# Optimization experiments

Measured on AMD Instinct MI355X. Metric: run time of the kernel, lower is better.

The kernel has to match this reference:

```python
import jax, jax.numpy as jnp
import numpy as np

B, N, P, K, E = 4, 20000, 128, 128, 160000


def setup_inputs() -> dict:
    key = jax.random.key(0)
    ks = jax.random.split(key, 16)
    inv_p = 1.0 / np.sqrt(P)
    inv_3p = 1.0 / np.sqrt(3 * P)
    return {
        "x_in": jax.random.normal(ks[0], (B, N, P), jnp.float32),
        "vertex_areas": jax.random.uniform(ks[1], (B, N), jnp.float32, 1e-3, 1.0),
        "evals": jax.random.uniform(ks[2], (B, K), jnp.float32, 0.0, 10.0),
        "evecs": jax.random.normal(ks[3], (B, N, K), jnp.float32),
        "gradX_vals": jax.random.normal(ks[4], (B, E), jnp.float32),
        "gradY_vals": jax.random.normal(ks[5], (B, E), jnp.float32),
        "grad_rows": jax.random.randint(ks[6], (B, E), 0, N, jnp.int32),
        "grad_cols": jax.random.randint(ks[7], (B, E), 0, N, jnp.int32),
        # learned params
        "diffusion_times": jax.random.uniform(ks[8], (P,), jnp.float32, 1e-3, 0.1),
        "B_re": jax.random.normal(ks[9], (P, P), jnp.float32) * inv_p,
        "B_im": jax.random.normal(ks[10], (P, P), jnp.float32) * inv_p,
        "W1": jax.random.normal(ks[11], (P, 3 * P), jnp.float32) * inv_3p,
        "b1": jnp.zeros((P,), jnp.float32),
        "W2": jax.random.normal(ks[12], (P, P), jnp.float32) * inv_p,
        "b2": jnp.zeros((P,), jnp.float32),
        "W3": jax.random.normal(ks[13], (P, P), jnp.float32) * inv_p,
        "b3": jnp.zeros((P,), jnp.float32),
    }


def _spmm(rows, cols, vals, x):
    # sparse (n,n) @ dense (n,p) via COO gather/scatter
    return jax.ops.segment_sum(vals[:, None] * x[cols], rows, num_segments=x.shape[0])


def reference(x_in, vertex_areas, evals, evecs, gradX_vals, gradY_vals,
              grad_rows, grad_cols, diffusion_times, B_re, B_im,
              W1, b1, W2, b2, W3, b3):
    # SpectralDiffusion: project -> spectral heat scaling -> unproject
    times = jnp.clip(diffusion_times, 1e-8)                       # (P,)
    x_spec = jnp.einsum('bnk,bnp->bkp', evecs, x_in * vertex_areas[..., None])
    scale = jnp.exp(-evals[..., None] * times[None, None, :])     # (B,K,P)
    x_diffuse = jnp.einsum('bnk,bkp->bnp', evecs, scale * x_spec)  # (B,N,P)

    # sparse gradient halves
    gx = jax.vmap(_spmm)(grad_rows, grad_cols, gradX_vals, x_diffuse)  # (B,N,P)
    gy = jax.vmap(_spmm)(grad_rows, grad_cols, gradY_vals, x_diffuse)

    # SpatialGradient: tanh(re*B_re(re) + im*B_im(im))
    x_grad_features = jnp.tanh(gx * (gx @ B_re.T) + gy * (gy @ B_im.T))

    # MiniMLP on concatenated features (dropout inactive in eval)
    h = jnp.concatenate([x_in, x_diffuse, x_grad_features], axis=-1)  # (B,N,3P)
    h = jax.nn.relu(h @ W1.T + b1)
    h = jax.nn.relu(h @ W2.T + b2)
    h = h @ W3.T + b3
    return h + x_in
```

## Files before the change

kernel.cpp:

```cpp
#include <hip/hip_runtime.h>
#include <hip/hip_bf16.h>
#include <cstddef>

#define B_ 4
#define N_ 20000
#define P_ 128
#define K_ 128
#define E_ 160000

constexpr int NCH_S = 79;
constexpr int NSCB  = 79;

typedef __attribute__((ext_vector_type(8))) short short8;
typedef __attribute__((ext_vector_type(4))) float f32x4;

__device__ __forceinline__ unsigned pk2(float x, float y) {
  __hip_bfloat162 h = __float22bfloat162_rn(make_float2(x, y));
  union { __hip_bfloat162 h; unsigned u; } c; c.h = h; return c.u;
}
__device__ __forceinline__ float bf2f(short s) {
  union { unsigned u; float f; } c; c.u = ((unsigned)(unsigned short)s) << 16; return c.f;
}

__global__ __launch_bounds__(256)
void k_prep(const float* __restrict__ ev, const float* __restrict__ xin,
            const float* __restrict__ areas,
            __hip_bfloat16* __restrict__ evT, __hip_bfloat16* __restrict__ xT)
{
  const int tn = blockIdx.x, half = blockIdx.y & 1, mat = blockIdx.y >> 1;
  const int b = blockIdx.z, t = threadIdx.x;
  const int n0 = tn * 64, c0 = half * 64;
  __shared__ float ld[64][65];
  const float* src = (mat ? xin : ev) + (size_t)b * N_ * 128;
  const float* ab  = areas + (size_t)b * N_;
#pragma unroll
  for (int i = 0; i < 4; ++i) {
    int gid = t + i * 256;
    int r = gid >> 4, c4 = (gid & 15) << 2;
    int n = n0 + r;
    float4 v = make_float4(0.f, 0.f, 0.f, 0.f);
    if (n < N_) {
      v = *(const float4*)(src + (size_t)n * 128 + c0 + c4);
      if (mat == 0) { float ar = ab[n]; v.x *= ar; v.y *= ar; v.z *= ar; v.w *= ar; }
    }
    ld[r][c4] = v.x; ld[r][c4+1] = v.y; ld[r][c4+2] = v.z; ld[r][c4+3] = v.w;
  }
  __syncthreads();
  __hip_bfloat16* dst = (mat ? xT : evT) + (size_t)b * 128 * N_;
#pragma unroll
  for (int i = 0; i < 4; ++i) {
    int gid = t + i * 256;
    int cr = gid >> 4, nq = (gid & 15) << 2;
    int n = n0 + nq;
    if (n + 4 <= N_) {
      uint2 u;
      u.x = pk2(ld[nq][cr],   ld[nq+1][cr]);
      u.y = pk2(ld[nq+2][cr], ld[nq+3][cr]);
      *(uint2*)(dst + (size_t)(c0 + cr) * N_ + n) = u;
    }
  }
}

__global__ __launch_bounds__(256)
void k_wprep(const float* __restrict__ Bre, const float* __restrict__ Bim,
             uint4* __restrict__ WfRe, uint4* __restrict__ WfIm)
{
  int fid = blockIdx.x * 256 + threadIdx.x;
  if (fid >= 2048) return;
  int gg = fid >> 7, rr = fid & 127;
  const float* s0 = Bre + rr * 128 + gg * 8;
  const float* s1 = Bim + rr * 128 + gg * 8;
  float4 a0 = *(const float4*)s0, a1 = *(const float4*)(s0 + 4);
  uint4 u; u.x = pk2(a0.x, a0.y); u.y = pk2(a0.z, a0.w);
  u.z = pk2(a1.x, a1.y); u.w = pk2(a1.z, a1.w);
  WfRe[fid] = u;
  float4 b0 = *(const float4*)s1, b1 = *(const float4*)(s1 + 4);
  uint4 v; v.x = pk2(b0.x, b0.y); v.y = pk2(b0.z, b0.w);
  v.z = pk2(b1.x, b1.y); v.w = pk2(b1.z, b1.w);
  WfIm[fid] = v;
}

__device__ __forceinline__ void stg64(uint4* __restrict__ Ls,
                                      const __hip_bfloat16* __restrict__ G,
                                      int n0, int t)
{
#pragma unroll
  for (int i = 0; i < 2; ++i) {
    int gid = t + i * 512;
    int r = gid >> 3, kg = gid & 7;
    int n = n0 + kg * 8;
    uint4 u = make_uint4(0u, 0u, 0u, 0u);
    if (n < N_) u = *(const uint4*)(G + (size_t)r * N_ + n);
    Ls[r * 8 + (kg ^ (r & 7))] = u;
  }
}

__global__ __launch_bounds__(512)
void k_spec_mm(const __hip_bfloat16* __restrict__ evT,
               const __hip_bfloat16* __restrict__ xT,
               float* __restrict__ part)
{
  const int c = blockIdx.x, b = blockIdx.y, t = threadIdx.x;
  const int l = t & 63, wid = t >> 6;
  const int wr = wid >> 2, wc = wid & 3;
  const int lr = l & 15, lg = l >> 4;
  __shared__ uint4 AsB[1024];
  __shared__ uint4 WsB[1024];
  f32x4 acc[4][2];
#pragma unroll
  for (int m = 0; m < 4; ++m)
#pragma unroll
    for (int n = 0; n < 2; ++n) acc[m][n] = (f32x4)0.f;

  const __hip_bfloat16* eb = evT + (size_t)b * 128 * N_;
  const __hip_bfloat16* xb = xT  + (size_t)b * 128 * N_;

  for (int s = 0; s < 4; ++s) {
    int n0 = c * 256 + s * 64;
    __syncthreads();
    stg64(AsB, eb, n0, t);
    stg64(WsB, xb, n0, t);
    __syncthreads();
    const short8* Ap = (const short8*)AsB;
    const short8* Wp = (const short8*)WsB;
#pragma unroll
    for (int kk = 0; kk < 2; ++kk) {
      int gg = kk * 4 + lg;
      short8 a[4], w[2];
#pragma unroll
      for (int m = 0; m < 4; ++m) { int rr = wr*64 + m*16 + lr; a[m] = Ap[rr*8 + (gg ^ (rr & 7))]; }
#pragma unroll
      for (int n = 0; n < 2; ++n) { int rr = wc*32 + n*16 + lr; w[n] = Wp[rr*8 + (gg ^ (rr & 7))]; }
#pragma unroll
      for (int m = 0; m < 4; ++m)
#pragma unroll
        for (int n = 0; n < 2; ++n)
          acc[m][n] = __builtin_amdgcn_mfma_f32_16x16x32_bf16(a[m], w[n], acc[m][n], 0, 0, 0);
    }
  }

  float* po = part + ((size_t)(b * NCH_S + c) << 14);
#pragma unroll
  for (int m = 0; m < 4; ++m)
#pragma unroll
    for (int r = 0; r < 4; ++r) {
      int row = wr*64 + m*16 + lg*4 + r;
#pragma unroll
      for (int n = 0; n < 2; ++n) {
        int col = wc*32 + n*16 + lr;
        po[row * 128 + col] = acc[m][n][r];
      }
    }
}

__global__ __launch_bounds__(256)
void k_spec_reduce(const float* __restrict__ partial, const float* __restrict__ evals,
                   const float* __restrict__ times, float* __restrict__ sspecT)
{
  int idx = blockIdx.x * 256 + threadIdx.x;
  int b = idx >> 14;
  int kp = idx & 16383;
  int k = kp >> 7, p = kp & 127;
  float s = 0.f;
  const float* pb = partial + (size_t)b * NCH_S * (K_*P_) + kp;
  for (int c = 0; c < NCH_S; ++c) s += pb[(size_t)c * (K_*P_)];
  float tt = times[p]; tt = tt < 1e-8f ? 1e-8f : tt;
  float sc = __expf(-evals[b*K_ + k] * tt);
  sspecT[((size_t)b*P_ + p) * K_ + k] = s * sc;
}

__device__ __forceinline__ void stg_f32(uint4* __restrict__ Ls, const float* __restrict__ G,
                                        int ld, int nrows, int t)
{
#pragma unroll
  for (int i = 0; i < 4; ++i) {
    int gid = t + i * 512;
    int r = gid >> 4, kg = gid & 15;
    float4 v0 = make_float4(0.f,0.f,0.f,0.f), v1 = v0;
    if (r < nrows) {
      const float* p = G + (size_t)r * ld + kg * 8;
      v0 = *(const float4*)p;
      v1 = *(const float4*)(p + 4);
    }
    uint4 u;
    u.x = pk2(v0.x, v0.y); u.y = pk2(v0.z, v0.w);
    u.z = pk2(v1.x, v1.y); u.w = pk2(v1.z, v1.w);
    Ls[r * 16 + (kg ^ (r & 7))] = u;
  }
}

__device__ __forceinline__ void stg_bf(uint4* __restrict__ Ls,
                                       const __hip_bfloat16* __restrict__ G,
                                       int ld, int nrows, int t)
{
#pragma unroll
  for (int i = 0; i < 4; ++i) {
    int gid = t + i * 512;
    int r = gid >> 4, kg = gid & 15;
    uint4 u = make_uint4(0u,0u,0u,0u);
    if (r < nrows) u = *(const uint4*)(G + (size_t)r * ld + kg * 8);
    Ls[r * 16 + (kg ^ (r & 7))] = u;
  }
}

__device__ __forceinline__ void mfma_chunk(const uint4* AsB, const uint4* WsB,
                                           int wr, int wc, int lr, int lg,
                                           f32x4 acc[4][2])
{
  const short8* Ap = (const short8*)AsB;
  const short8* Wp = (const short8*)WsB;
#pragma unroll
  for (int kk = 0; kk < 4; ++kk) {
    int gg = kk * 4 + lg;
    short8 a[4], w[2];
#pragma unroll
    for (int m = 0; m < 4; ++m) {
      int rr = wr*64 + m*16 + lr;
      a[m] = Ap[rr*16 + (gg ^ (rr & 7))];
    }
#pragma unroll
    for (int n = 0; n < 2; ++n) {
      int rr = wc*32 + n*16 + lr;
      w[n] = Wp[rr*16 + (gg ^ (rr & 7))];
    }
#pragma unroll
    for (int m = 0; m < 4; ++m)
#pragma unroll
      for (int n = 0; n < 2; ++n)
        acc[m][n] = __builtin_amdgcn_mfma_f32_16x16x32_bf16(a[m], w[n], acc[m][n], 0, 0, 0);
  }
}

template<int MODE>
__global__ __launch_bounds__(512)
void k_rowgemm(const void* __restrict__ A0, const void* __restrict__ A1,
               const void* __restrict__ A2, int abf,
               const float* __restrict__ W, int ldw, int wbs, int nchunk,
               const float* __restrict__ bias, const float* __restrict__ resid,
               void* __restrict__ C)
{
  const int b = blockIdx.y, r0 = blockIdx.x * 128, t = threadIdx.x;
  const int l = t & 63, wid = t >> 6;
  const int wr = wid >> 2, wc = wid & 3;
  const int lr = l & 15, lg = l >> 4;
  __shared__ uint4 AsB[2048];
  __shared__ uint4 WsB[2048];
  f32x4 acc[4][2];
#pragma unroll
  for (int m = 0; m < 4; ++m)
#pragma unroll
    for (int n = 0; n < 2; ++n) acc[m][n] = (f32x4)0.f;

  const float* Wb = W + (size_t)b * wbs;
  const int nrows = min(128, N_ - r0);
  const size_t aoff = (size_t)b * N_ * 128 + (size_t)r0 * 128;

  for (int kc = 0; kc < nchunk; ++kc) {
    const void* Av = (kc == 0 ? A0 : (kc == 1 ? A1 : A2));
    __syncthreads();
    if ((abf >> kc) & 1) stg_bf(AsB, (const __hip_bfloat16*)Av + aoff, 128, nrows, t);
    else                 stg_f32(AsB, (const float*)Av + aoff, 128, nrows, t);
    stg_f32(WsB, Wb + kc * 128, ldw, 128, t);
    __syncthreads();
    mfma_chunk(AsB, WsB, wr, wc, lr, lg, acc);
  }

  const size_t cb = (size_t)b * N_ * 128;
#pragma unroll
  for (int m = 0; m < 4; ++m) {
    int rowt = wr*64 + m*16 + lg*4;
#pragma unroll
    for (int r = 0; r < 4; ++r) {
      int row = r0 + rowt + r;
      if (row >= N_) continue;
#pragma unroll
      for (int n = 0; n < 2; ++n) {
        int col = wc*32 + n*16 + lr;
        float v = acc[m][n][r];
        if (MODE == 1 || MODE == 2) v = fmaxf(v + bias[col], 0.f);
        if (MODE == 3) {
          v += bias[col] + resid[cb + (size_t)row*128 + col];
          ((float*)C)[cb + (size_t)row*128 + col] = v;
        } else {
          ((__hip_bfloat16*)C)[cb + (size_t)row*128 + col] = __float2bfloat16(v);
        }
      }
    }
  }
}

__device__ __forceinline__ void stg64r(uint4* __restrict__ Ls,
                                       const __hip_bfloat16* __restrict__ G,
                                       int nrows, int t)
{
#pragma unroll
  for (int i = 0; i < 4; ++i) {
    int gid = t + i * 256;
    int r = gid >> 4, kg = gid & 15;
    uint4 u = make_uint4(0u,0u,0u,0u);
    if (r < nrows) u = *(const uint4*)(G + (size_t)r * 128 + kg * 8);
    Ls[r * 16 + (kg ^ (r & 7))] = u;
  }
}

__device__ __forceinline__ void mfma_pass64(const uint4* As, const uint4* __restrict__ Wf,
                                            int wc, int lr, int lg, f32x4 acc[4][2])
{
  const short8* Ap = (const short8*)As;
  const short8* Wp = (const short8*)Wf;
#pragma unroll
  for (int kk = 0; kk < 4; ++kk) {
    int gg = kk * 4 + lg;
    short8 a[4], w[2];
#pragma unroll
    for (int m = 0; m < 4; ++m) { int rr = m*16 + lr; a[m] = Ap[rr*16 + (gg ^ (rr & 7))]; }
#pragma unroll
    for (int n = 0; n < 2; ++n) { int rr = wc*32 + n*16 + lr; w[n] = Wp[(gg << 7) + rr]; }
#pragma unroll
    for (int m = 0; m < 4; ++m)
#pragma unroll
      for (int n = 0; n < 2; ++n)
        acc[m][n] = __builtin_amdgcn_mfma_f32_16x16x32_bf16(a[m], w[n], acc[m][n], 0, 0, 0);
  }
}

__global__ __launch_bounds__(256)
void k_grad(const uint4* __restrict__ WfRe, const uint4* __restrict__ WfIm,
            __hip_bfloat16* __restrict__ gx, const __hip_bfloat16* __restrict__ gy)
{
  const int b = blockIdx.y, r0 = blockIdx.x * 64, t = threadIdx.x;
  const int l = t & 63, wc = t >> 6;
  const int lr = l & 15, lg = l >> 4;
  __shared__ uint4 As[1024];
  f32x4 acc1[4][2], acc2[4][2];
#pragma unroll
  for (int m = 0; m < 4; ++m)
#pragma unroll
    for (int n = 0; n < 2; ++n) { acc1[m][n] = (f32x4)0.f; acc2[m][n] = (f32x4)0.f; }

  __hip_bfloat16*       gxb = gx + (size_t)b * N_ * P_;
  const __hip_bfloat16* gyb = gy + (size_t)b * N_ * P_;
  const int nrows = min(64, N_ - r0);

  stg64r(As, gxb + (size_t)r0 * 128, nrows, t);
  __syncthreads();
  mfma_pass64(As, WfRe, wc, lr, lg, acc1);
  __syncthreads();
  stg64r(As, gyb + (size_t)r0 * 128, nrows, t);
#pragma unroll
  for (int m = 0; m < 4; ++m)
#pragma unroll
    for (int r = 0; r < 4; ++r) {
      int row = r0 + m*16 + lg*4 + r;
      if (row >= N_) continue;
#pragma unroll
      for (int n = 0; n < 2; ++n) {
        int col = wc*32 + n*16 + lr;
        acc1[m][n][r] *= bf2f(*(const short*)(gxb + (size_t)row*128 + col));
      }
    }
  __syncthreads();
  mfma_pass64(As, WfIm, wc, lr, lg, acc2);

#pragma unroll
  for (int m = 0; m < 4; ++m)
#pragma unroll
    for (int r = 0; r < 4; ++r) {
      int row = r0 + m*16 + lg*4 + r;
      if (row >= N_) continue;
#pragma unroll
      for (int n = 0; n < 2; ++n) {
        int col = wc*32 + n*16 + lr;
        float g2 = bf2f(*(const short*)(gyb + (size_t)row*128 + col));
        float s = acc1[m][n][r] + g2 * acc2[m][n][r];
        s = fminf(fmaxf(s, -15.f), 15.f);
        float e = __expf(2.f * s);
        gxb[(size_t)row*128 + col] = __float2bfloat16((e - 1.f) / (e + 1.f));
      }
    }
}

__global__ void k_count(const int* __restrict__ rows, int* __restrict__ cnt)
{
  int b = blockIdx.y;
  int e = blockIdx.x * 256 + threadIdx.x;
  if (e < E_) atomicAdd(&cnt[b*N_ + rows[(size_t)b*E_ + e]], 1);
}

__global__ __launch_bounds__(256)
void k_scan_blk(const int* __restrict__ cnt, int* __restrict__ off,
                int* __restrict__ bsum)
{
  const int c = blockIdx.x, b = blockIdx.y, t = threadIdx.x;
  const int lane = t & 63, wid = t >> 6;
  __shared__ int wt[4];
  int i = c * 256 + t;
  int v = (i < N_) ? cnt[b*N_ + i] : 0;
  int x = v;
#pragma unroll
  for (int ofs = 1; ofs < 64; ofs <<= 1) {
    int y = __shfl_up(x, ofs, 64);
    if (lane >= ofs) x += y;
  }
  if (lane == 63) wt[wid] = x;
  __syncthreads();
  int wofs = 0;
  for (int wj = 0; wj < wid; ++wj) wofs += wt[wj];
  if (i < N_) off[b*(N_+1) + i] = wofs + x - v;
  if (t == 255) bsum[b*128 + c] = wofs + x;
}

__global__ __launch_bounds__(64)
void k_scan_top(int* __restrict__ bsum, int* __restrict__ off)
{
  const int b = blockIdx.x, t = threadIdx.x;
  int running = 0;
  for (int base = 0; base < 128; base += 64) {
    int i = base + t;
    int v = (i < NSCB) ? bsum[b*128 + i] : 0;
    int x = v;
#pragma unroll
    for (int ofs = 1; ofs < 64; ofs <<= 1) {
      int y = __shfl_up(x, ofs, 64);
      if (t >= ofs) x += y;
    }
    if (i < 128) bsum[b*128 + i] = running + x - v;
    running += __shfl(x, 63, 64);
  }
  if (t == 0) off[b*(N_+1) + N_] = running;
}

__global__ __launch_bounds__(256)
void k_scan_add(const int* __restrict__ bsum, int* __restrict__ off,
                int* __restrict__ pos)
{
  const int c = blockIdx.x, b = blockIdx.y;
  int i = c * 256 + (int)threadIdx.x;
  if (i < N_) {
    int o = off[b*(N_+1) + i] + bsum[b*128 + c];
    off[b*(N_+1) + i] = o;
    pos[b*N_ + i] = o;
  }
}

__global__ void k_fill(const int* __restrict__ rows, const int* __restrict__ cols,
                       const float* __restrict__ vx, const float* __restrict__ vy,
                       int* __restrict__ pos, uint4* __restrict__ prec)
{
  int b = blockIdx.y;
  int e = blockIdx.x * 256 + threadIdx.x;
  if (e < E_) {
    size_t be = (size_t)b*E_ + e;
    int r = rows[be];
    int p = atomicAdd(&pos[b*N_ + r], 1);
    if (p >= 0 && p < E_) {
      uint4 rec;
      rec.x = (unsigned)cols[be];
      rec.y = __float_as_uint(vx[be]);
      rec.z = __float_as_uint(vy[be]);
      rec.w = 0u;
      prec[(size_t)b*E_ + p] = rec;
    }
  }
}

__global__ __launch_bounds__(256)
void k_gather(const __hip_bfloat16* __restrict__ xd, const uint4* __restrict__ prec,
              const int* __restrict__ off,
              __hip_bfloat16* __restrict__ gx, __hip_bfloat16* __restrict__ gy)
{
  const int b = blockIdx.y;
  const int row = (blockIdx.x * 256 + threadIdx.x) >> 6;
  const int lane = threadIdx.x & 63;
  const int q = lane >> 4, ql = lane & 15;
  if (row >= N_) return;
  const int s = off[b*(N_+1) + row], e = off[b*(N_+1) + row + 1];
  float ax[8], ay[8];
#pragma unroll
  for (int k = 0; k < 8; ++k) { ax[k] = 0.f; ay[k] = 0.f; }
  const __hip_bfloat16* xdb = xd + (size_t)b * N_ * P_;
  const uint4* pb = prec + (size_t)b * E_;

  for (int i = s; i < e; i += 4) {
    int idx = i + q;
    bool valid = idx < e;
    uint4 rec = pb[valid ? idx : (e - 1)];
    float fx = valid ? __uint_as_float(rec.y) : 0.f;
    float fy = valid ? __uint_as_float(rec.z) : 0.f;
    uint4 v = *(const uint4*)(xdb + (size_t)rec.x * P_ + ql * 8);
    float x0 = __uint_as_float(v.x << 16), x1 = __uint_as_float(v.x & 0xffff0000u);
    float x2 = __uint_as_float(v.y << 16), x3 = __uint_as_float(v.y & 0xffff0000u);
    float x4 = __uint_as_float(v.z << 16), x5 = __uint_as_float(v.z & 0xffff0000u);
    float x6 = __uint_as_float(v.w << 16), x7 = __uint_as_float(v.w & 0xffff0000u);
    ax[0] = fmaf(fx, x0, ax[0]); ax[1] = fmaf(fx, x1, ax[1]);
    ax[2] = fmaf(fx, x2, ax[2]); ax[3] = fmaf(fx, x3, ax[3]);
    ax[4] = fmaf(fx, x4, ax[4]); ax[5] = fmaf(fx, x5, ax[5]);
    ax[6] = fmaf(fx, x6, ax[6]); ax[7] = fmaf(fx, x7, ax[7]);
    ay[0] = fmaf(fy, x0, ay[0]); ay[1] = fmaf(fy, x1, ay[1]);
    ay[2] = fmaf(fy, x2, ay[2]); ay[3] = fmaf(fy, x3, ay[3]);
    ay[4] = fmaf(fy, x4, ay[4]); ay[5] = fmaf(fy, x5, ay[5]);
    ay[6] = fmaf(fy, x6, ay[6]); ay[7] = fmaf(fy, x7, ay[7]);
  }
#pragma unroll
  for (int k = 0; k < 8; ++k) {
    ax[k] += __shfl_xor(ax[k], 16, 64); ax[k] += __shfl_xor(ax[k], 32, 64);
    ay[k] += __shfl_xor(ay[k], 16, 64); ay[k] += __shfl_xor(ay[k], 32, 64);
  }
  if (lane < 16) {
    size_t o = (size_t)b * N_ * P_ + (size_t)row * P_ + ql * 8;
    uint4 ux, uy;
    ux.x = pk2(ax[0], ax[1]); ux.y = pk2(ax[2], ax[3]);
    ux.z = pk2(ax[4], ax[5]); ux.w = pk2(ax[6], ax[7]);
    uy.x = pk2(ay[0], ay[1]); uy.y = pk2(ay[2], ay[3]);
    uy.z = pk2(ay[4], ay[5]); uy.w = pk2(ay[6], ay[7]);
    *(uint4*)(gx + o) = ux;
    *(uint4*)(gy + o) = uy;
  }
}

extern "C" void kernel_launch(void* const* d_in, const int* in_sizes, int n_in,
                              void* d_out, int out_size, void* d_ws, size_t ws_size,
                              hipStream_t stream)
{
  const float* x_in  = (const float*)d_in[0];
  const float* areas = (const float*)d_in[1];
  const float* evals = (const float*)d_in[2];
  const float* evecs = (const float*)d_in[3];
  const float* gXv   = (const float*)d_in[4];
  const float* gYv   = (const float*)d_in[5];
  const int*   grows = (const int*)d_in[6];
  const int*   gcols = (const int*)d_in[7];
  const float* times = (const float*)d_in[8];
  const float* Bre   = (const float*)d_in[9];
  const float* Bim   = (const float*)d_in[10];
  const float* W1    = (const float*)d_in[11];
  const float* b1    = (const float*)d_in[12];
  const float* W2    = (const float*)d_in[13];
  const float* b2    = (const float*)d_in[14];
  const float* W3    = (const float*)d_in[15];
  const float* b3    = (const float*)d_in[16];

  float* ws = (float*)d_ws;
  __hip_bfloat16* xd_bf = (__hip_bfloat16*)ws;
  float*          part  = ws + 6000000;
  __hip_bfloat16* gx_bf = (__hip_bfloat16*)(ws + 12000000);
  __hip_bfloat16* gy_bf = (__hip_bfloat16*)(ws + 18000000);
  __hip_bfloat16* evT   = gx_bf;
  __hip_bfloat16* xT    = gy_bf;

  uint4* prec   = (uint4*)(ws + 24000000);
  int*   ipos   = (int*)(ws + 26560000);
  int*   ioff   = ipos + B_*N_;
  float* sspecT = ws + 26750000;
  uint4* WfRe   = (uint4*)(ws + 26816000);
  uint4* WfIm   = WfRe + 2048;
  int*   bsum   = (int*)(WfIm + 2048);
  float* out    = (float*)d_out;

  const int GB = (N_ + 127) / 128;
  const int TN = (N_ + 63) / 64;

  k_prep<<<dim3(TN, 4, B_), 256, 0, stream>>>(evecs, x_in, areas, evT, xT);
  k_wprep<<<dim3(8), 256, 0, stream>>>(Bre, Bim, WfRe, WfIm);
  k_spec_mm<<<dim3(NCH_S, B_), 512, 0, stream>>>(evT, xT, part);
  k_spec_reduce<<<dim3(B_*K_*P_/256), 256, 0, stream>>>(part, evals, times, sspecT);
  k_rowgemm<0><<<dim3(GB, B_), 512, 0, stream>>>(evecs, nullptr, nullptr, 0, sspecT,
                                                 128, K_*P_, 1, nullptr, nullptr, xd_bf);
  hipMemsetAsync(ipos, 0, (size_t)B_*N_*sizeof(int), stream);
  k_count<<<dim3(E_/256, B_), 256, 0, stream>>>(grows, ipos);
  k_scan_blk<<<dim3(NSCB, B_), 256, 0, stream>>>(ipos, ioff, bsum);
  k_scan_top<<<dim3(B_), 64, 0, stream>>>(bsum, ioff);
  k_scan_add<<<dim3(NSCB, B_), 256, 0, stream>>>(bsum, ioff, ipos);
  k_fill<<<dim3(E_/256, B_), 256, 0, stream>>>(grows, gcols, gXv, gYv, ipos, prec);
  k_gather<<<dim3(N_/4, B_), 256, 0, stream>>>(xd_bf, prec, ioff, gx_bf, gy_bf);
  k_grad<<<dim3(TN, B_), 256, 0, stream>>>(WfRe, WfIm, gx_bf, gy_bf);
  k_rowgemm<1><<<dim3(GB, B_), 512, 0, stream>>>(x_in, xd_bf, gx_bf, 0b110, W1,
                                                 384, 0, 3, b1, nullptr, gy_bf);
  k_rowgemm<2><<<dim3(GB, B_), 512, 0, stream>>>(gy_bf, nullptr, nullptr, 1, W2,
                                                 128, 0, 1, b2, nullptr, gx_bf);
  k_rowgemm<3><<<dim3(GB, B_), 512, 0, stream>>>(gx_bf, nullptr, nullptr, 1, W3,
                                                 128, 0, 1, b3, x_in, out);
}
```

Measured before the change: 274.8 us.

## Fuse sparse gradient gather with spatial-gradient MFMA kernel via LDS staging

```diff
diff --git a/kernel.cpp b/kernel.cpp
--- a/kernel.cpp
+++ b/kernel.cpp
@@ -289,20 +289,6 @@
   }
 }
 
-__device__ __forceinline__ void stg64r(uint4* __restrict__ Ls,
-                                       const __hip_bfloat16* __restrict__ G,
-                                       int nrows, int t)
-{
-#pragma unroll
-  for (int i = 0; i < 4; ++i) {
-    int gid = t + i * 256;
-    int r = gid >> 4, kg = gid & 15;
-    uint4 u = make_uint4(0u,0u,0u,0u);
-    if (r < nrows) u = *(const uint4*)(G + (size_t)r * 128 + kg * 8);
-    Ls[r * 16 + (kg ^ (r & 7))] = u;
-  }
-}
-
 __device__ __forceinline__ void mfma_pass64(const uint4* As, const uint4* __restrict__ Wf,
                                             int wc, int lr, int lg, f32x4 acc[4][2])
 {
@@ -325,57 +311,95 @@
 }
 
 __global__ __launch_bounds__(256)
-void k_grad(const uint4* __restrict__ WfRe, const uint4* __restrict__ WfIm,
-            __hip_bfloat16* __restrict__ gx, const __hip_bfloat16* __restrict__ gy)
+void k_gather_grad(const __hip_bfloat16* __restrict__ xd, const uint4* __restrict__ prec,
+                   const int* __restrict__ off,
+                   const uint4* __restrict__ WfRe, const uint4* __restrict__ WfIm,
+                   __hip_bfloat16* __restrict__ xg)
 {
   const int b = blockIdx.y, r0 = blockIdx.x * 64, t = threadIdx.x;
-  const int l = t & 63, wc = t >> 6;
+  const int l = t & 63, w = t >> 6;
+  const int q = l >> 4, ql = l & 15;
+  __shared__ uint4 As[1024];
+  __shared__ uint4 As2[1024];
+  const __hip_bfloat16* xdb = xd + (size_t)b * N_ * P_;
+  const uint4* pb = prec + (size_t)b * E_;
+
+  for (int rr = 0; rr < 16; ++rr) {
+    const int lrow = w * 16 + rr;
+    const int row = r0 + lrow;
+    if (row < N_) {
+      const int s = off[b*(N_+1) + row], e = off[b*(N_+1) + row + 1];
+      float ax[8], ay[8];
+#pragma unroll
+      for (int k = 0; k < 8; ++k) { ax[k] = 0.f; ay[k] = 0.f; }
+      for (int i = s; i < e; i += 4) {
+        int idx = i + q;
+        bool valid = idx < e;
+        uint4 rec = pb[valid ? idx : (e - 1)];
+        float fx = valid ? __uint_as_float(rec.y) : 0.f;
+        float fy = valid ? __uint_as_float(rec.z) : 0.f;
+        uint4 v = *(const uint4*)(xdb + (size_t)rec.x * P_ + ql * 8);
+        float x0 = __uint_as_float(v.x << 16), x1 = __uint_as_float(v.x & 0xffff0000u);
+        float x2 = __uint_as_float(v.y << 16), x3 = __uint_as_float(v.y & 0xffff0000u);
+        float x4 = __uint_as_float(v.z << 16), x5 = __uint_as_float(v.z & 0xffff0000u);
+        float x6 = __uint_as_float(v.w << 16), x7 = __uint_as_float(v.w & 0xffff0000u);
+        ax[0] = fmaf(fx, x0, ax[0]); ax[1] = fmaf(fx, x1, ax[1]);
+        ax[2] = fmaf(fx, x2, ax[2]); ax[3] = fmaf(fx, x3, ax[3]);
+        ax[4] = fmaf(fx, x4, ax[4]); ax[5] = fmaf(fx, x5, ax[5]);
+        ax[6] = fmaf(fx, x6, ax[6]); ax[7] = fmaf(fx, x7, ax[7]);
+        ay[0] = fmaf(fy, x0, ay[0]); ay[1] = fmaf(fy, x1, ay[1]);
+        ay[2] = fmaf(fy, x2, ay[2]); ay[3] = fmaf(fy, x3, ay[3]);
+        ay[4] = fmaf(fy, x4, ay[4]); ay[5] = fmaf(fy, x5, ay[5]);
+        ay[6] = fmaf(fy, x6, ay[6]); ay[7] = fmaf(fy, x7, ay[7]);
+      }
+#pragma unroll
+      for (int k = 0; k < 8; ++k) {
+        ax[k] += __shfl_xor(ax[k], 16, 64); ax[k] += __shfl_xor(ax[k], 32, 64);
+        ay[k] += __shfl_xor(ay[k], 16, 64); ay[k] += __shfl_xor(ay[k], 32, 64);
+      }
+      if (l < 16) {
+        int sidx = lrow * 16 + (ql ^ (lrow & 7));
+        uint4 ux, uy;
+        ux.x = pk2(ax[0], ax[1]); ux.y = pk2(ax[2], ax[3]);
+        ux.z = pk2(ax[4], ax[5]); ux.w = pk2(ax[6], ax[7]);
+        uy.x = pk2(ay[0], ay[1]); uy.y = pk2(ay[2], ay[3]);
+        uy.z = pk2(ay[4], ay[5]); uy.w = pk2(ay[6], ay[7]);
+        As[sidx] = ux;
+        As2[sidx] = uy;
+      }
+    }
+  }
+  __syncthreads();
+
   const int lr = l & 15, lg = l >> 4;
-  __shared__ uint4 As[1024];
   f32x4 acc1[4][2], acc2[4][2];
 #pragma unroll
   for (int m = 0; m < 4; ++m)
 #pragma unroll
     for (int n = 0; n < 2; ++n) { acc1[m][n] = (f32x4)0.f; acc2[m][n] = (f32x4)0.f; }
-
-  __hip_bfloat16*       gxb = gx + (size_t)b * N_ * P_;
-  const __hip_bfloat16* gyb = gy + (size_t)b * N_ * P_;
-  const int nrows = min(64, N_ - r0);
-
-  stg64r(As, gxb + (size_t)r0 * 128, nrows, t);
-  __syncthreads();
-  mfma_pass64(As, WfRe, wc, lr, lg, acc1);
-  __syncthreads();
-  stg64r(As, gyb + (size_t)r0 * 128, nrows, t);
+  mfma_pass64(As,  WfRe, w, lr, lg, acc1);
+  mfma_pass64(As2, WfIm, w, lr, lg, acc2);
+
+  const short* S1 = (const short*)As;
+  const short* S2 = (const short*)As2;
+  __hip_bfloat16* xgb = xg + (size_t)b * N_ * P_;
 #pragma unroll
   for (int m = 0; m < 4; ++m)
 #pragma unroll
     for (int r = 0; r < 4; ++r) {
-      int row = r0 + m*16 + lg*4 + r;
+      int rowt = m*16 + lg*4 + r;
+      int row = r0 + rowt;
       if (row >= N_) continue;
 #pragma unroll
       for (int n = 0; n < 2; ++n) {
-        int col = wc*32 + n*16 + lr;
-        acc1[m][n][r] *= bf2f(*(const short*)(gxb + (size_t)row*128 + col));
-      }
-    }
-  __syncthreads();
-  mfma_pass64(As, WfIm, wc, lr, lg, acc2);
-
-#pragma unroll
-  for (int m = 0; m < 4; ++m)
-#pragma unroll
-    for (int r = 0; r < 4; ++r) {
-      int row = r0 + m*16 + lg*4 + r;
-      if (row >= N_) continue;
-#pragma unroll
-      for (int n = 0; n < 2; ++n) {
-        int col = wc*32 + n*16 + lr;
-        float g2 = bf2f(*(const short*)(gyb + (size_t)row*128 + col));
-        float s = acc1[m][n][r] + g2 * acc2[m][n][r];
+        int col = w*32 + n*16 + lr;
+        int gidx = (rowt*16 + ((col>>3) ^ (rowt & 7)))*8 + (col & 7);
+        float g1 = bf2f(S1[gidx]);
+        float g2 = bf2f(S2[gidx]);
+        float s = g1 * acc1[m][n][r] + g2 * acc2[m][n][r];
         s = fminf(fmaxf(s, -15.f), 15.f);
         float e = __expf(2.f * s);
-        gxb[(size_t)row*128 + col] = __float2bfloat16((e - 1.f) / (e + 1.f));
+        xgb[(size_t)row*128 + col] = __float2bfloat16((e - 1.f) / (e + 1.f));
       }
     }
 }
@@ -461,60 +485,6 @@
       rec.w = 0u;
       prec[(size_t)b*E_ + p] = rec;
     }
-  }
-}
-
-__global__ __launch_bounds__(256)
-void k_gather(const __hip_bfloat16* __restrict__ xd, const uint4* __restrict__ prec,
-              const int* __restrict__ off,
-              __hip_bfloat16* __restrict__ gx, __hip_bfloat16* __restrict__ gy)
-{
-  const int b = blockIdx.y;
-  const int row = (blockIdx.x * 256 + threadIdx.x) >> 6;
-  const int lane = threadIdx.x & 63;
-  const int q = lane >> 4, ql = lane & 15;
-  if (row >= N_) return;
-  const int s = off[b*(N_+1) + row], e = off[b*(N_+1) + row + 1];
-  float ax[8], ay[8];
-#pragma unroll
-  for (int k = 0; k < 8; ++k) { ax[k] = 0.f; ay[k] = 0.f; }
-  const __hip_bfloat16* xdb = xd + (size_t)b * N_ * P_;
-  const uint4* pb = prec + (size_t)b * E_;
-
-  for (int i = s; i < e; i += 4) {
-    int idx = i + q;
-    bool valid = idx < e;
-    uint4 rec = pb[valid ? idx : (e - 1)];
-    float fx = valid ? __uint_as_float(rec.y) : 0.f;
-    float fy = valid ? __uint_as_float(rec.z) : 0.f;
-    uint4 v = *(const uint4*)(xdb + (size_t)rec.x * P_ + ql * 8);
-    float x0 = __uint_as_float(v.x << 16), x1 = __uint_as_float(v.x & 0xffff0000u);
-    float x2 = __uint_as_float(v.y << 16), x3 = __uint_as_float(v.y & 0xffff0000u);
-    float x4 = __uint_as_float(v.z << 16), x5 = __uint_as_float(v.z & 0xffff0000u);
-    float x6 = __uint_as_float(v.w << 16), x7 = __uint_as_float(v.w & 0xffff0000u);
-    ax[0] = fmaf(fx, x0, ax[0]); ax[1] = fmaf(fx, x1, ax[1]);
-    ax[2] = fmaf(fx, x2, ax[2]); ax[3] = fmaf(fx, x3, ax[3]);
-    ax[4] = fmaf(fx, x4, ax[4]); ax[5] = fmaf(fx, x5, ax[5]);
-    ax[6] = fmaf(fx, x6, ax[6]); ax[7] = fmaf(fx, x7, ax[7]);
-    ay[0] = fmaf(fy, x0, ay[0]); ay[1] = fmaf(fy, x1, ay[1]);
-    ay[2] = fmaf(fy, x2, ay[2]); ay[3] = fmaf(fy, x3, ay[3]);
-    ay[4] = fmaf(fy, x4, ay[4]); ay[5] = fmaf(fy, x5, ay[5]);
-    ay[6] = fmaf(fy, x6, ay[6]); ay[7] = fmaf(fy, x7, ay[7]);
-  }
-#pragma unroll
-  for (int k = 0; k < 8; ++k) {
-    ax[k] += __shfl_xor(ax[k], 16, 64); ax[k] += __shfl_xor(ax[k], 32, 64);
-    ay[k] += __shfl_xor(ay[k], 16, 64); ay[k] += __shfl_xor(ay[k], 32, 64);
-  }
-  if (lane < 16) {
-    size_t o = (size_t)b * N_ * P_ + (size_t)row * P_ + ql * 8;
-    uint4 ux, uy;
-    ux.x = pk2(ax[0], ax[1]); ux.y = pk2(ax[2], ax[3]);
-    ux.z = pk2(ax[4], ax[5]); ux.w = pk2(ax[6], ax[7]);
-    uy.x = pk2(ay[0], ay[1]); uy.y = pk2(ay[2], ay[3]);
-    uy.z = pk2(ay[4], ay[5]); uy.w = pk2(ay[6], ay[7]);
-    *(uint4*)(gx + o) = ux;
-    *(uint4*)(gy + o) = uy;
   }
 }
 
@@ -572,8 +542,8 @@
   k_scan_top<<<dim3(B_), 64, 0, stream>>>(bsum, ioff);
   k_scan_add<<<dim3(NSCB, B_), 256, 0, stream>>>(bsum, ioff, ipos);
   k_fill<<<dim3(E_/256, B_), 256, 0, stream>>>(grows, gcols, gXv, gYv, ipos, prec);
-  k_gather<<<dim3(N_/4, B_), 256, 0, stream>>>(xd_bf, prec, ioff, gx_bf, gy_bf);
-  k_grad<<<dim3(TN, B_), 256, 0, stream>>>(WfRe, WfIm, gx_bf, gy_bf);
+  k_gather_grad<<<dim3(TN, B_), 256, 0, stream>>>(xd_bf, prec, ioff, WfRe, WfIm,
+                                                  gx_bf);
   k_rowgemm<1><<<dim3(GB, B_), 512, 0, stream>>>(x_in, xd_bf, gx_bf, 0b110, W1,
                                                  384, 0, 3, b1, nullptr, gy_bf);
   k_rowgemm<2><<<dim3(GB, B_), 512, 0, stream>>>(gy_bf, nullptr, nullptr, 1, W2,
```

Result: slower. 294.4 us (+7.1%).
